# Kernel tuning notes

Measured on AMD Instinct MI355X. Metric: run time of the kernel, lower is better.

The kernel has to match this reference:

```python
import jax, jax.numpy as jnp
import numpy as np

N, L, D = 1024, 128, 512
H = D // 2  # LSTM hidden per direction


def _lstm_dir(x, w_ih, w_hh, b_ih, b_hh, reverse=False):
    # x: [B, T, Din] -> [B, T, H]; PyTorch gate order i, f, g, o
    B = x.shape[0]
    Hh = w_hh.shape[1]
    xs = jnp.swapaxes(x, 0, 1)  # [T, B, Din]
    if reverse:
        xs = xs[::-1]
    pre = jnp.einsum('tbi,gi->tbg', xs, w_ih) + b_ih  # precompute input contribution

    def step(carry, p):
        h, c = carry
        g = p + h @ w_hh.T + b_hh
        i, f, cc, o = jnp.split(g, 4, axis=-1)
        c = jax.nn.sigmoid(f) * c + jax.nn.sigmoid(i) * jnp.tanh(cc)
        h = jax.nn.sigmoid(o) * jnp.tanh(c)
        return (h, c), h

    zeros = jnp.zeros((B, Hh), x.dtype)
    _, hs = jax.lax.scan(step, (zeros, zeros), pre)
    if reverse:
        hs = hs[::-1]
    return jnp.swapaxes(hs, 0, 1)


def _bilstm(x, params):
    # params: [(w_ih, w_hh, b_ih, b_hh)] for l0_fwd, l0_bwd, l1_fwd, l1_bwd
    for lf, lb in ((params[0], params[1]), (params[2], params[3])):
        f = _lstm_dir(x, *lf)
        b = _lstm_dir(x, *lb, reverse=True)
        x = jnp.concatenate([f, b], axis=-1)
    return x


def _forward(episodes, query, current_state, ages, Wq, bq, Wk, bk, lstm_params, k):
    # retrieve_relevant_episodes: batched version of the per-episode loop
    query_proj = query @ Wq.T + bq              # [D]
    emb = episodes.mean(axis=1)                 # [N, D] per-episode mean embedding
    key_proj = emb @ Wk.T + bk                  # [N, D]
    scores = key_proj @ query_proj              # [N] (matmul(q, kp.T).mean() == dot for 1D)
    _, idx = jax.lax.top_k(scores, k)           # descending, == argsort[-k:][::-1]
    sel = jnp.take(episodes, idx, axis=0)       # [k, L, D]
    # temporal_attention
    w = 1.0 / (1.0 + jnp.take(ages, idx) * 0.01)  # temporal recency weight
    x = sel * w[:, None, None]
    lstm_out = _bilstm(x, lstm_params)          # [k, L, D]
    att = jnp.einsum('d,kld->kl', current_state, lstm_out)  # [k, L] (== [k,1,L])
    attw = jax.nn.softmax(att, axis=-1)
    context = jnp.einsum('kl,kld->kd', attw, lstm_out)[:, None, :]  # [k, 1, D]
    return context


def setup_inputs() -> dict:
    key = jax.random.key(0)
    ks = jax.random.split(key, 32)
    s = 1.0 / np.sqrt(D)
    sh = 1.0 / np.sqrt(H)
    inp = {
        'episodes': jax.random.normal(ks[0], (N, L, D), jnp.float32),
        'query': jax.random.normal(ks[1], (D,), jnp.float32),
        'current_state': jax.random.normal(ks[2], (D,), jnp.float32),
        'ages': jax.random.uniform(ks[3], (N,), jnp.float32) * 100.0,
        'Wq': jax.random.normal(ks[4], (D, D), jnp.float32) * s,
        'bq': jnp.zeros((D,), jnp.float32),
        'Wk': jax.random.normal(ks[5], (D, D), jnp.float32) * s,
        'bk': jnp.zeros((D,), jnp.float32),
    }
    i = 6
    for name in ['l0', 'l0r', 'l1', 'l1r']:
        inp['w_ih_' + name] = jax.random.normal(ks[i], (4 * H, D), jnp.float32) * sh; i += 1
        inp['w_hh_' + name] = jax.random.normal(ks[i], (4 * H, H), jnp.float32) * sh; i += 1
        inp['b_ih_' + name] = jnp.zeros((4 * H,), jnp.float32)
        inp['b_hh_' + name] = jnp.zeros((4 * H,), jnp.float32)
    inp['k'] = 5
    return inp


def reference(episodes, query, current_state, ages, Wq, bq, Wk, bk,
              w_ih_l0, w_hh_l0, b_ih_l0, b_hh_l0,
              w_ih_l0r, w_hh_l0r, b_ih_l0r, b_hh_l0r,
              w_ih_l1, w_hh_l1, b_ih_l1, b_hh_l1,
              w_ih_l1r, w_hh_l1r, b_ih_l1r, b_hh_l1r, k):
    lstm_params = [
        (w_ih_l0, w_hh_l0, b_ih_l0, b_hh_l0),
        (w_ih_l0r, w_hh_l0r, b_ih_l0r, b_hh_l0r),
        (w_ih_l1, w_hh_l1, b_ih_l1, b_hh_l1),
        (w_ih_l1r, w_hh_l1r, b_ih_l1r, b_hh_l1r),
    ]
    return _forward(episodes, query, current_state, ages, Wq, bq, Wk, bk, lstm_params, k)
```

## Files before the change

kernel.cpp:

```cpp
#include <hip/hip_runtime.h>
#include <hip/hip_bf16.h>
#include <math.h>

typedef unsigned short u16;
typedef unsigned int   u32;
typedef unsigned long long u64;

#define DEV static __device__ __forceinline__

static constexpr int LL = 128, DD = 512, HH = 256, KK = 5, NN = 1024;

static constexpr size_t OFF_QP   = 0;
static constexpr size_t OFF_U    = 4096;
static constexpr size_t OFF_CC   = 8192;
static constexpr size_t OFF_SC   = 12288;
static constexpr size_t OFF_WSC  = 16384;
static constexpr size_t OFF_IDX  = 16640;
static constexpr size_t OFF_HG   = 20480;
static constexpr size_t OFF_FLG0 = 61440;
static constexpr size_t OFF_FLG1 = 65536;
static constexpr size_t OFF_PRE  = 73728;
static constexpr size_t OFF_OUT0 = OFF_PRE  + (size_t)2*LL*5*1024*4;
static constexpr size_t OFF_OUT1 = OFF_OUT0 + (size_t)5*LL*DD*4;

DEV float sigf(float x){ return 1.0f/(1.0f + expf(-x)); }

__global__ void k_qproj(const float* __restrict__ Wq, const float* __restrict__ q,
                        const float* __restrict__ bq, float* __restrict__ qp) {
  __shared__ float qs[512];
  int tid = threadIdx.x;
  qs[tid] = q[tid]; qs[tid+256] = q[tid+256];
  __syncthreads();
  int row  = blockIdx.x*8 + (tid >> 5);
  int lane = tid & 31;
  const float* wr = Wq + (size_t)row*512 + lane*16;
  float acc = 0.f;
  #pragma unroll
  for (int j = 0; j < 16; j += 4) {
    float4 w = *(const float4*)(wr + j);
    acc += w.x*qs[lane*16+j] + w.y*qs[lane*16+j+1] + w.z*qs[lane*16+j+2] + w.w*qs[lane*16+j+3];
  }
  #pragma unroll
  for (int off = 16; off > 0; off >>= 1) acc += __shfl_down(acc, off, 32);
  if (lane == 0) qp[row] = acc + bq[row];
}

__global__ void k_keyvec(const float* __restrict__ Wk, const float* __restrict__ bk,
                         const float* __restrict__ qp, float* __restrict__ u,
                         float* __restrict__ cconst) {
  __shared__ float qs[512];
  __shared__ float red[16][17];
  __shared__ float r2[256];
  int tid = threadIdx.x;
  qs[tid] = qp[tid]; qs[tid+256] = qp[tid+256];
  __syncthreads();
  int cl = tid & 15;
  int jc = tid >> 4;
  int col = blockIdx.x*16 + cl;
  float acc = 0.f;
  for (int j = jc*32; j < jc*32 + 32; ++j) acc += Wk[(size_t)j*512 + col] * qs[j];
  red[cl][jc] = acc;
  __syncthreads();
  if (tid < 16) {
    float a = 0.f;
    #pragma unroll
    for (int m = 0; m < 16; ++m) a += red[tid][m];
    u[blockIdx.x*16 + tid] = a;
  }
  if (blockIdx.x == 0) {
    float b2 = bk[tid]*qs[tid] + bk[tid+256]*qs[tid+256];
    r2[tid] = b2;
    __syncthreads();
    for (int off = 128; off > 0; off >>= 1) { if (tid < off) r2[tid] += r2[tid+off]; __syncthreads(); }
    if (tid == 0) cconst[0] = r2[0];
  }
}

__global__ void k_scores(const float* __restrict__ ep, const float* __restrict__ u,
                         const float* __restrict__ cconst, float* __restrict__ scores) {
  __shared__ float red[256];
  int tid = threadIdx.x, n = blockIdx.x;
  int d0 = (tid * 4) & 511;
  float u0 = u[d0+0], u1 = u[d0+1], u2 = u[d0+2], u3 = u[d0+3];
  const float* base = ep + (size_t)n * (LL*DD);
  float acc = 0.f;
  for (int c = tid; c < (LL*DD)/4; c += 256) {
    float4 v = *(const float4*)(base + (size_t)c*4);
    acc += v.x*u0 + v.y*u1 + v.z*u2 + v.w*u3;
  }
  red[tid] = acc;
  __syncthreads();
  for (int off = 128; off > 0; off >>= 1) { if (tid < off) red[tid] += red[tid+off]; __syncthreads(); }
  if (tid == 0) scores[n] = red[0] * (1.0f/LL) + cconst[0];
}

__global__ void k_topk(const float* __restrict__ scores, const float* __restrict__ ages,
                       int* __restrict__ idx5, float* __restrict__ wsc) {
  __shared__ float s0[NN];
  __shared__ float sv[NN];
  __shared__ int   si[NN];
  __shared__ int   chosen[KK];
  int tid = threadIdx.x;
  s0[tid] = scores[tid];
  __syncthreads();
  for (int r = 0; r < KK; ++r) {
    float v = s0[tid];
    for (int m = 0; m < r; ++m) if (chosen[m] == tid) v = -3.4e38f;
    sv[tid] = v; si[tid] = tid;
    __syncthreads();
    for (int off = 512; off > 0; off >>= 1) {
      if (tid < off) {
        float a = sv[tid], b = sv[tid+off];
        int ia = si[tid], ib = si[tid+off];
        if (b > a || (b == a && ib < ia)) { sv[tid] = b; si[tid] = ib; }
      }
      __syncthreads();
    }
    if (tid == 0) {
      int w = si[0];
      chosen[r] = w;
      idx5[r] = w;
      wsc[r] = 1.0f / (1.0f + ages[w] * 0.01f);
    }
    __syncthreads();
  }
}

__global__ __launch_bounds__(256) void k_pre(
    const float* __restrict__ ep, const float* __restrict__ x1,
    const int* __restrict__ idx5, const float* __restrict__ wsc,
    const float* __restrict__ wihF, const float* __restrict__ wihB,
    const float* __restrict__ bihF, const float* __restrict__ bhhF,
    const float* __restrict__ bihB, const float* __restrict__ bhhB,
    float* __restrict__ pre) {
  int t = blockIdx.x, dir = blockIdx.y;
  int tid = threadIdx.x;
  __shared__ __align__(16) float xs[5*512];
  if (ep) {
    for (int f = tid; f < 5*512; f += 256) {
      int b = f >> 9, i = f & 511;
      xs[f] = ep[((size_t)idx5[b]*LL + t)*DD + i] * wsc[b];
    }
  } else {
    for (int f = tid; f < 5*512; f += 256) {
      int b = f >> 9, i = f & 511;
      xs[f] = x1[((size_t)b*LL + t)*DD + i];
    }
  }
  const float* wih = dir ? wihB : wihF;
  const float* bih = dir ? bihB : bihF;
  const float* bhh = dir ? bhhB : bhhF;
  __syncthreads();

  const float4* w4 = (const float4*)wih;
  const float4* x4 = (const float4*)xs;
  float acc[4][5];
  #pragma unroll
  for (int g = 0; g < 4; ++g)
    #pragma unroll
    for (int b = 0; b < 5; ++b) acc[g][b] = 0.f;

  #pragma unroll 4
  for (int kq = 0; kq < 128; ++kq) {
    float4 xv[5];
    #pragma unroll
    for (int b = 0; b < 5; ++b) xv[b] = x4[b*128 + kq];
    #pragma unroll
    for (int g = 0; g < 4; ++g) {
      float4 w = w4[(size_t)(tid + g*256)*128 + kq];
      #pragma unroll
      for (int b = 0; b < 5; ++b) {
        acc[g][b] += w.x*xv[b].x + w.y*xv[b].y + w.z*xv[b].z + w.w*xv[b].w;
      }
    }
  }

  size_t pbase = (((size_t)dir*LL + t)*5)*1024;
  #pragma unroll
  for (int g = 0; g < 4; ++g) {
    int row = tid + g*256;
    float bias = bih[row] + bhh[row];
    #pragma unroll
    for (int b = 0; b < 5; ++b)
      pre[pbase + (size_t)b*1024 + row] = acc[g][b] + bias;
  }
}

__global__ __launch_bounds__(1024) void k_lstm(
    const float* __restrict__ whhF, const float* __restrict__ whhB,
    const float* __restrict__ pre, float* __restrict__ out,
    float* __restrict__ hg, int* __restrict__ flg) {
  int wg  = blockIdx.x;
  int dir = wg >> 3;
  int q   = wg & 7;
  int tid = threadIdx.x;
  int rp  = tid & 63;
  int jq  = tid >> 6;
  int jb  = jq * 16;
  const float* whh = dir ? whhB : whhF;

  __shared__ __align__(16) float h_lds[5*256];
  __shared__ __align__(16) float part[5*16*130];
  __shared__ float c_s[5*32];
  __shared__ float pre_lds[5*128];

  int r0 = 2*rp, r1 = 2*rp + 1;
  int gr0 = (r0 >> 5)*256 + q*32 + (r0 & 31);
  int gr1 = (r1 >> 5)*256 + q*32 + (r1 & 31);
  float w0[16], w1[16];
  #pragma unroll
  for (int m4 = 0; m4 < 4; ++m4) {
    float4 a = *(const float4*)(whh + (size_t)gr0*256 + jb + m4*4);
    w0[m4*4+0]=a.x; w0[m4*4+1]=a.y; w0[m4*4+2]=a.z; w0[m4*4+3]=a.w;
    float4 c = *(const float4*)(whh + (size_t)gr1*256 + jb + m4*4);
    w1[m4*4+0]=c.x; w1[m4*4+1]=c.y; w1[m4*4+2]=c.z; w1[m4*4+3]=c.w;
  }
  for (int f = tid; f < 1280; f += 1024) h_lds[f] = 0.f;
  if (tid < 160) c_s[tid] = 0.f;
  float* hg_dir = hg + (size_t)dir * 2 * 1280;
  int*  flg_dir = flg + dir * 64;
  __syncthreads();

  for (int s = 0; s < LL; ++s) {
    int t = dir ? (LL-1-s) : s;
    if (tid < 640) {
      int b = tid >> 7, r = tid & 127;
      int grow = (r >> 5)*256 + q*32 + (r & 31);
      pre_lds[tid] = pre[(((size_t)dir*LL + t)*5 + b)*1024 + grow];
    }
    if (s > 0) {
      const float* hrd = hg_dir + (size_t)(s & 1) * 1280;
      if (tid < 8) {
        while (__hip_atomic_load(&flg_dir[tid], __ATOMIC_RELAXED,
                                 __HIP_MEMORY_SCOPE_AGENT) < s) {}
      }
      __syncthreads();
      for (int f = tid; f < 1120; f += 1024) {
        int b = f / 224, w2 = f % 224;
        int c7 = w2 >> 5, u = w2 & 31;
        int pch = c7 + (c7 >= q);
        int idx = b*256 + pch*32 + u;
        h_lds[idx] = __hip_atomic_load(&hrd[idx], __ATOMIC_RELAXED,
                                       __HIP_MEMORY_SCOPE_AGENT);
      }
    }
    __syncthreads();
    {
      float acc0[5], acc1[5];
      #pragma unroll
      for (int b = 0; b < 5; ++b) {
        const float4* h4 = (const float4*)&h_lds[b*256 + jb];
        float a0 = 0.f, a1 = 0.f;
        #pragma unroll
        for (int m4 = 0; m4 < 4; ++m4) {
          float4 hv = h4[m4];
          a0 += w0[m4*4+0]*hv.x + w0[m4*4+1]*hv.y + w0[m4*4+2]*hv.z + w0[m4*4+3]*hv.w;
          a1 += w1[m4*4+0]*hv.x + w1[m4*4+1]*hv.y + w1[m4*4+2]*hv.z + w1[m4*4+3]*hv.w;
        }
        acc0[b] = a0; acc1[b] = a1;
      }
      #pragma unroll
      for (int b = 0; b < 5; ++b) {
        *(float2*)&part[(b*16 + jq)*130 + 2*rp] = make_float2(acc0[b], acc1[b]);
      }
    }
    __syncthreads();
    if (tid < 160) {
      int b = tid >> 5, u = tid & 31;
      float g[4];
      #pragma unroll
      for (int gate = 0; gate < 4; ++gate) {
        int r = gate*32 + u;
        float sum = pre_lds[b*128 + r];
        #pragma unroll
        for (int m = 0; m < 16; ++m) sum += part[(b*16 + m)*130 + r];
        g[gate] = sum;
      }
      float ig = sigf(g[0]), fg = sigf(g[1]), cc = tanhf(g[2]), og = sigf(g[3]);
      float cn = fg * c_s[b*32 + u] + ig * cc;
      c_s[b*32 + u] = cn;
      float hv = og * tanhf(cn);
      out[((size_t)b*LL + t)*DD + dir*HH + q*32 + u] = hv;
      h_lds[b*256 + q*32 + u] = hv;
      float* hwr = hg_dir + (size_t)((s + 1) & 1) * 1280;
      __hip_atomic_store(&hwr[b*256 + q*32 + u], hv,
                         __ATOMIC_RELAXED, __HIP_MEMORY_SCOPE_AGENT);
    }
    __syncthreads();
    if (tid == 0)
      __hip_atomic_store(&flg_dir[q], s + 1, __ATOMIC_RELAXED,
                         __HIP_MEMORY_SCOPE_AGENT);
  }
}

__global__ void k_attn(const float* __restrict__ out1, const float* __restrict__ csb,
                       float* __restrict__ outp) {
  int b = blockIdx.x, tid = threadIdx.x;
  __shared__ float cs[512];
  __shared__ float att[128];
  __shared__ float red[256];
  __shared__ float smax, ssum;
  cs[tid] = csb[tid]; cs[tid+256] = csb[tid+256];
  __syncthreads();
  {
    int t = tid & 127, half = tid >> 7;
    const float* row = out1 + ((size_t)b*LL + t)*DD + half*256;
    const float* c2 = cs + half*256;
    float a = 0.f;
    for (int d = 0; d < 256; ++d) a += row[d] * c2[d];
    red[tid] = a;
  }
  __syncthreads();
  if (tid < 128) att[tid] = red[tid] + red[tid+128];
  __syncthreads();
  if (tid < 64) red[tid] = fmaxf(att[tid], att[tid+64]);
  __syncthreads();
  if (tid == 0) { float m = red[0]; for (int o = 1; o < 64; ++o) m = fmaxf(m, red[o]); smax = m; }
  __syncthreads();
  if (tid < 128) att[tid] = expf(att[tid] - smax);
  __syncthreads();
  if (tid < 64) red[tid] = att[tid] + att[tid+64];
  __syncthreads();
  if (tid == 0) { float s = 0.f; for (int o = 0; o < 64; ++o) s += red[o]; ssum = s; }
  __syncthreads();
  float inv = 1.0f / ssum;
  for (int d = tid; d < DD; d += 256) {
    float acc = 0.f;
    for (int t2 = 0; t2 < LL; ++t2) acc += att[t2] * out1[((size_t)b*LL + t2)*DD + d];
    outp[b*DD + d] = acc * inv;
  }
}

extern "C" void kernel_launch(void* const* d_in, const int* in_sizes, int n_in,
                              void* d_out, int out_size, void* d_ws, size_t ws_size,
                              hipStream_t stream) {
  (void)in_sizes; (void)n_in; (void)out_size; (void)ws_size;
  const float* ep   = (const float*)d_in[0];
  const float* qu   = (const float*)d_in[1];
  const float* cst  = (const float*)d_in[2];
  const float* ages = (const float*)d_in[3];
  const float* Wq   = (const float*)d_in[4];
  const float* bq   = (const float*)d_in[5];
  const float* Wk   = (const float*)d_in[6];
  const float* bk   = (const float*)d_in[7];
  const float *wih[4], *whh[4], *bih[4], *bhh[4];
  for (int l = 0; l < 4; ++l) {
    wih[l] = (const float*)d_in[8 + l*4 + 0];
    whh[l] = (const float*)d_in[8 + l*4 + 1];
    bih[l] = (const float*)d_in[8 + l*4 + 2];
    bhh[l] = (const float*)d_in[8 + l*4 + 3];
  }
  char* ws = (char*)d_ws;
  float* qp   = (float*)(ws + OFF_QP);
  float* uvec = (float*)(ws + OFF_U);
  float* cc   = (float*)(ws + OFF_CC);
  float* sc   = (float*)(ws + OFF_SC);
  float* wsc  = (float*)(ws + OFF_WSC);
  int*   idx5 = (int*)  (ws + OFF_IDX);
  float* hg0  = (float*)(ws + OFF_HG);
  float* hg1  = (float*)(ws + OFF_HG + 20480);
  int*   flg0 = (int*)  (ws + OFF_FLG0);
  int*   flg1 = (int*)  (ws + OFF_FLG1);
  float* pre  = (float*)(ws + OFF_PRE);
  float* out0 = (float*)(ws + OFF_OUT0);
  float* out1 = (float*)(ws + OFF_OUT1);

  hipMemsetAsync(ws + OFF_FLG0, 0, 8192, stream);

  k_qproj <<<64, 256, 0, stream>>>(Wq, qu, bq, qp);
  k_keyvec<<<32, 256, 0, stream>>>(Wk, bk, qp, uvec, cc);
  k_scores<<<NN, 256, 0, stream>>>(ep, uvec, cc, sc);
  k_topk  <<<1, 1024, 0, stream>>>(sc, ages, idx5, wsc);

  k_pre <<<dim3(LL,2), 256, 0, stream>>>(ep, nullptr, idx5, wsc,
        wih[0], wih[1], bih[0], bhh[0], bih[1], bhh[1], pre);
  k_lstm<<<16, 1024, 0, stream>>>(whh[0], whh[1], pre, out0, hg0, flg0);

  k_pre <<<dim3(LL,2), 256, 0, stream>>>(nullptr, out0, idx5, wsc,
        wih[2], wih[3], bih[2], bhh[2], bih[3], bhh[3], pre);
  k_lstm<<<16, 1024, 0, stream>>>(whh[2], whh[3], pre, out1, hg1, flg1);

  k_attn<<<KK, 256, 0, stream>>>(out1, cst, (float*)d_out);
}
```

Before: 1.435 ms.

## Fuse front-end projection, scoring and top-k into one kernel with atomic counters

```diff
diff --git a/kernel.cpp b/kernel.cpp
--- a/kernel.cpp
+++ b/kernel.cpp
@@ -19,110 +19,145 @@
 static constexpr size_t OFF_HG   = 20480;
 static constexpr size_t OFF_FLG0 = 61440;
 static constexpr size_t OFF_FLG1 = 65536;
+static constexpr size_t OFF_CNT  = 69632;
 static constexpr size_t OFF_PRE  = 73728;
 static constexpr size_t OFF_OUT0 = OFF_PRE  + (size_t)2*LL*5*1024*4;
 static constexpr size_t OFF_OUT1 = OFF_OUT0 + (size_t)5*LL*DD*4;
 
 DEV float sigf(float x){ return 1.0f/(1.0f + expf(-x)); }
 
-__global__ void k_qproj(const float* __restrict__ Wq, const float* __restrict__ q,
-                        const float* __restrict__ bq, float* __restrict__ qp) {
+DEV float ald(const float* p) {
+  return __hip_atomic_load(p, __ATOMIC_RELAXED, __HIP_MEMORY_SCOPE_AGENT);
+}
+DEV void ast(float* p, float v) {
+  __hip_atomic_store(p, v, __ATOMIC_RELAXED, __HIP_MEMORY_SCOPE_AGENT);
+}
+template<int SLP>
+DEV void wait_ge(int* p, int v) {
+  while (__hip_atomic_load(p, __ATOMIC_RELAXED, __HIP_MEMORY_SCOPE_AGENT) < v)
+    __builtin_amdgcn_s_sleep(SLP);
+}
+
+__global__ __launch_bounds__(256) void k_front(
+    const float* __restrict__ Wq, const float* __restrict__ qu,
+    const float* __restrict__ bq, const float* __restrict__ Wk,
+    const float* __restrict__ bk, const float* __restrict__ ep,
+    const float* __restrict__ ages,
+    float* __restrict__ qp, float* __restrict__ u, float* __restrict__ cconst,
+    float* __restrict__ scores, int* __restrict__ idx5, float* __restrict__ wsc,
+    int* __restrict__ cnt) {
   __shared__ float qs[512];
-  int tid = threadIdx.x;
-  qs[tid] = q[tid]; qs[tid+256] = q[tid+256];
-  __syncthreads();
-  int row  = blockIdx.x*8 + (tid >> 5);
-  int lane = tid & 31;
-  const float* wr = Wq + (size_t)row*512 + lane*16;
-  float acc = 0.f;
-  #pragma unroll
-  for (int j = 0; j < 16; j += 4) {
-    float4 w = *(const float4*)(wr + j);
-    acc += w.x*qs[lane*16+j] + w.y*qs[lane*16+j+1] + w.z*qs[lane*16+j+2] + w.w*qs[lane*16+j+3];
-  }
-  #pragma unroll
-  for (int off = 16; off > 0; off >>= 1) acc += __shfl_down(acc, off, 32);
-  if (lane == 0) qp[row] = acc + bq[row];
-}
-
-__global__ void k_keyvec(const float* __restrict__ Wk, const float* __restrict__ bk,
-                         const float* __restrict__ qp, float* __restrict__ u,
-                         float* __restrict__ cconst) {
-  __shared__ float qs[512];
-  __shared__ float red[16][17];
+  __shared__ float red2[16][17];
   __shared__ float r2[256];
-  int tid = threadIdx.x;
-  qs[tid] = qp[tid]; qs[tid+256] = qp[tid+256];
-  __syncthreads();
-  int cl = tid & 15;
-  int jc = tid >> 4;
-  int col = blockIdx.x*16 + cl;
-  float acc = 0.f;
-  for (int j = jc*32; j < jc*32 + 32; ++j) acc += Wk[(size_t)j*512 + col] * qs[j];
-  red[cl][jc] = acc;
-  __syncthreads();
-  if (tid < 16) {
-    float a = 0.f;
-    #pragma unroll
-    for (int m = 0; m < 16; ++m) a += red[tid][m];
-    u[blockIdx.x*16 + tid] = a;
-  }
-  if (blockIdx.x == 0) {
-    float b2 = bk[tid]*qs[tid] + bk[tid+256]*qs[tid+256];
-    r2[tid] = b2;
-    __syncthreads();
-    for (int off = 128; off > 0; off >>= 1) { if (tid < off) r2[tid] += r2[tid+off]; __syncthreads(); }
-    if (tid == 0) cconst[0] = r2[0];
-  }
-}
-
-__global__ void k_scores(const float* __restrict__ ep, const float* __restrict__ u,
-                         const float* __restrict__ cconst, float* __restrict__ scores) {
-  __shared__ float red[256];
-  int tid = threadIdx.x, n = blockIdx.x;
-  int d0 = (tid * 4) & 511;
-  float u0 = u[d0+0], u1 = u[d0+1], u2 = u[d0+2], u3 = u[d0+3];
-  const float* base = ep + (size_t)n * (LL*DD);
-  float acc = 0.f;
-  for (int c = tid; c < (LL*DD)/4; c += 256) {
-    float4 v = *(const float4*)(base + (size_t)c*4);
-    acc += v.x*u0 + v.y*u1 + v.z*u2 + v.w*u3;
-  }
-  red[tid] = acc;
-  __syncthreads();
-  for (int off = 128; off > 0; off >>= 1) { if (tid < off) red[tid] += red[tid+off]; __syncthreads(); }
-  if (tid == 0) scores[n] = red[0] * (1.0f/LL) + cconst[0];
-}
-
-__global__ void k_topk(const float* __restrict__ scores, const float* __restrict__ ages,
-                       int* __restrict__ idx5, float* __restrict__ wsc) {
+  __shared__ float redS[256];
   __shared__ float s0[NN];
-  __shared__ float sv[NN];
-  __shared__ int   si[NN];
+  __shared__ float sv[256];
+  __shared__ int   si[256];
   __shared__ int   chosen[KK];
-  int tid = threadIdx.x;
-  s0[tid] = scores[tid];
-  __syncthreads();
-  for (int r = 0; r < KK; ++r) {
-    float v = s0[tid];
-    for (int m = 0; m < r; ++m) if (chosen[m] == tid) v = -3.4e38f;
-    sv[tid] = v; si[tid] = tid;
-    __syncthreads();
-    for (int off = 512; off > 0; off >>= 1) {
-      if (tid < off) {
-        float a = sv[tid], b = sv[tid+off];
-        int ia = si[tid], ib = si[tid+off];
-        if (b > a || (b == a && ib < ia)) { sv[tid] = b; si[tid] = ib; }
-      }
+  int bid = blockIdx.x, tid = threadIdx.x;
+
+  if (bid < 64) {
+    qs[tid] = qu[tid]; qs[tid+256] = qu[tid+256];
+    __syncthreads();
+    int row = bid*8 + (tid >> 5), lane = tid & 31;
+    const float* wr = Wq + (size_t)row*512 + lane*16;
+    float acc = 0.f;
+    #pragma unroll
+    for (int j = 0; j < 16; j += 4) {
+      float4 w = *(const float4*)(wr + j);
+      acc += w.x*qs[lane*16+j] + w.y*qs[lane*16+j+1] + w.z*qs[lane*16+j+2] + w.w*qs[lane*16+j+3];
+    }
+    #pragma unroll
+    for (int off = 16; off > 0; off >>= 1) acc += __shfl_down(acc, off, 32);
+    if (lane == 0) ast(&qp[row], acc + bq[row]);
+    __syncthreads();
+    if (tid == 0) __hip_atomic_fetch_add(&cnt[0], 1, __ATOMIC_RELAXED, __HIP_MEMORY_SCOPE_AGENT);
+    __syncthreads();
+  }
+
+  if (bid >= 64 && bid < 96) {
+    if (tid == 0) wait_ge<2>(&cnt[0], 64);
+    __syncthreads();
+    qs[tid] = ald(&qp[tid]); qs[tid+256] = ald(&qp[tid+256]);
+    __syncthreads();
+    int kb = bid - 64;
+    int cl = tid & 15, jc = tid >> 4;
+    int col = kb*16 + cl;
+    float acc = 0.f;
+    for (int j = jc*32; j < jc*32 + 32; ++j) acc += Wk[(size_t)j*512 + col] * qs[j];
+    red2[cl][jc] = acc;
+    __syncthreads();
+    if (tid < 16) {
+      float a = 0.f;
+      #pragma unroll
+      for (int m = 0; m < 16; ++m) a += red2[tid][m];
+      ast(&u[kb*16 + tid], a);
+    }
+    if (kb == 0) {
+      float b2 = bk[tid]*qs[tid] + bk[tid+256]*qs[tid+256];
+      r2[tid] = b2;
       __syncthreads();
-    }
-    if (tid == 0) {
-      int w = si[0];
-      chosen[r] = w;
-      idx5[r] = w;
-      wsc[r] = 1.0f / (1.0f + ages[w] * 0.01f);
-    }
-    __syncthreads();
+      for (int off = 128; off > 0; off >>= 1) { if (tid < off) r2[tid] += r2[tid+off]; __syncthreads(); }
+      if (tid == 0) ast(&cconst[0], r2[0]);
+    }
+    __syncthreads();
+    if (tid == 0) __hip_atomic_fetch_add(&cnt[1], 1, __ATOMIC_RELAXED, __HIP_MEMORY_SCOPE_AGENT);
+    __syncthreads();
+  }
+
+  {
+    if (tid == 0) wait_ge<32>(&cnt[1], 32);
+    __syncthreads();
+    int d0 = (tid * 4) & 511;
+    float u0 = ald(&u[d0+0]), u1 = ald(&u[d0+1]), u2 = ald(&u[d0+2]), u3 = ald(&u[d0+3]);
+    float ccv = ald(cconst);
+    const float* base = ep + (size_t)bid * (LL*DD);
+    float acc = 0.f;
+    for (int c = tid; c < (LL*DD)/4; c += 256) {
+      float4 v = *(const float4*)(base + (size_t)c*4);
+      acc += v.x*u0 + v.y*u1 + v.z*u2 + v.w*u3;
+    }
+    redS[tid] = acc;
+    __syncthreads();
+    for (int off = 128; off > 0; off >>= 1) { if (tid < off) redS[tid] += redS[tid+off]; __syncthreads(); }
+    if (tid == 0) ast(&scores[bid], redS[0] * (1.0f/LL) + ccv);
+    __syncthreads();
+    if (tid == 0) __hip_atomic_fetch_add(&cnt[2], 1, __ATOMIC_RELAXED, __HIP_MEMORY_SCOPE_AGENT);
+  }
+
+  if (bid == 0) {
+    if (tid == 0) wait_ge<8>(&cnt[2], NN);
+    __syncthreads();
+    #pragma unroll
+    for (int k = 0; k < 4; ++k) s0[tid + k*256] = ald(&scores[tid + k*256]);
+    __syncthreads();
+    for (int r = 0; r < KK; ++r) {
+      float bv = -3.4e38f; int bi = 0x7fffffff;
+      #pragma unroll
+      for (int k = 0; k < 4; ++k) {
+        int i = tid + k*256;
+        float v = s0[i];
+        bool excl = false;
+        for (int m = 0; m < r; ++m) excl = excl || (chosen[m] == i);
+        if (!excl && (v > bv || (v == bv && i < bi))) { bv = v; bi = i; }
+      }
+      sv[tid] = bv; si[tid] = bi;
+      __syncthreads();
+      for (int off = 128; off > 0; off >>= 1) {
+        if (tid < off) {
+          float b = sv[tid+off]; int ib = si[tid+off];
+          if (b > sv[tid] || (b == sv[tid] && ib < si[tid])) { sv[tid] = b; si[tid] = ib; }
+        }
+        __syncthreads();
+      }
+      if (tid == 0) {
+        int w = si[0];
+        chosen[r] = w;
+        idx5[r] = w;
+        wsc[r] = 1.0f / (1.0f + ages[w] * 0.01f);
+      }
+      __syncthreads();
+    }
   }
 }
 
@@ -361,16 +396,15 @@
   float* hg1  = (float*)(ws + OFF_HG + 20480);
   int*   flg0 = (int*)  (ws + OFF_FLG0);
   int*   flg1 = (int*)  (ws + OFF_FLG1);
+  int*   cnt  = (int*)  (ws + OFF_CNT);
   float* pre  = (float*)(ws + OFF_PRE);
   float* out0 = (float*)(ws + OFF_OUT0);
   float* out1 = (float*)(ws + OFF_OUT1);
 
-  hipMemsetAsync(ws + OFF_FLG0, 0, 8192, stream);
-
-  k_qproj <<<64, 256, 0, stream>>>(Wq, qu, bq, qp);
-  k_keyvec<<<32, 256, 0, stream>>>(Wk, bk, qp, uvec, cc);
-  k_scores<<<NN, 256, 0, stream>>>(ep, uvec, cc, sc);
-  k_topk  <<<1, 1024, 0, stream>>>(sc, ages, idx5, wsc);
+  (void)hipMemsetAsync(ws + OFF_FLG0, 0, 12288, stream);
+
+  k_front<<<NN, 256, 0, stream>>>(Wq, qu, bq, Wk, bk, ep, ages,
+                                  qp, uvec, cc, sc, idx5, wsc, cnt);
 
   k_pre <<<dim3(LL,2), 256, 0, stream>>>(ep, nullptr, idx5, wsc,
         wih[0], wih[1], bih[0], bhh[0], bih[1], bhh[1], pre);
```

New measurement: 1.443 ms. About the same (+0.6%).
